# Kernel optimization log

Hardware: AMD Instinct MI355X
Metric: run time of the kernel (lower is better)

Reference implementation:

```python
import jax, jax.numpy as jnp
import numpy as np

E = 1024
H = 16
HD = E // H  # 64


def setup_inputs() -> dict:
    key = jax.random.key(0)
    ks = jax.random.split(key, 5)
    x = jax.random.normal(ks[0], (2, 2048, E), dtype=jnp.float32)
    s = 1.0 / np.sqrt(E)
    W_qkv = jax.random.uniform(ks[1], (E, 3 * E), jnp.float32, -s, s)
    b_qkv = jax.random.uniform(ks[2], (3 * E,), jnp.float32, -s, s)
    W_out = jax.random.uniform(ks[3], (E, E), jnp.float32, -s, s)
    b_out = jax.random.uniform(ks[4], (E,), jnp.float32, -s, s)
    return {"x": x, "W_qkv": W_qkv, "b_qkv": b_qkv, "W_out": W_out, "b_out": b_out}


def reference(x, W_qkv, b_qkv, W_out, b_out):
    B, N, _ = x.shape
    scale = HD ** (-0.5)
    qkv = x @ W_qkv + b_qkv                         # [B, N, 3E]
    qkv = qkv.reshape(B, N, H, 3 * HD)              # torch layout: per-head 3*hd chunk
    qkv = qkv.transpose(0, 2, 1, 3)                 # [B, H, N, 3*hd]
    q, k, v = jnp.split(qkv, 3, axis=-1)            # each [B, H, N, hd]
    attn = jnp.einsum('bhqd,bhkd->bhqk', q, k) * scale
    attn = jax.nn.softmax(attn, axis=-1)            # dropout is identity in eval
    out = jnp.einsum('bhqk,bhkd->bhqd', attn, v)    # [B, H, N, hd]
    out = out.transpose(0, 2, 1, 3).reshape(B, N, E)
    return out @ W_out + b_out
```

## Files before the change

kernel.cpp:

```cpp
#include <hip/hip_runtime.h>


#define SEQ 2048
#define NH  16

typedef __attribute__((ext_vector_type(8))) short short8;
typedef __attribute__((ext_vector_type(4))) short short4v;
typedef __attribute__((ext_vector_type(4))) float floatx4;
typedef __attribute__((ext_vector_type(4))) _Float16 half4;
typedef __attribute__((ext_vector_type(8))) _Float16 half8;
typedef __attribute__((ext_vector_type(2))) _Float16 half2v;
typedef __attribute__((ext_vector_type(2))) __fp16 fp16x2;

#define QSCALE 0.1803368801111204f

__device__ __forceinline__ short f2bf(float f) {
    union { float f; unsigned u; } v; v.f = f;
    unsigned r = v.u + 0x7fffu + ((v.u >> 16) & 1u);
    return (short)(r >> 16);
}

__device__ __forceinline__ float fast_exp2(float x) {
#if __has_builtin(__builtin_amdgcn_exp2f)
    return __builtin_amdgcn_exp2f(x);
#else
    return exp2f(x);
#endif
}

__device__ __forceinline__ half2v cvt_pk(float a, float b) {
#if __has_builtin(__builtin_amdgcn_cvt_pkrtz)
    union { fp16x2 i; half2v o; } u;
    u.i = __builtin_amdgcn_cvt_pkrtz(a, b);
    return u.o;
#else
    half2v r; r.x = (_Float16)a; r.y = (_Float16)b; return r;
#endif
}

#define GLDS16(gp, lp)                                                          \
    __builtin_amdgcn_global_load_lds(                                           \
        (const __attribute__((address_space(1))) unsigned int*)(gp),            \
        (__attribute__((address_space(3))) unsigned int*)(lp), 16, 0, 0)

__global__ __launch_bounds__(256) void prep_kernel(
    const float* __restrict__ x,  short* __restrict__ xb,
    const float* __restrict__ wq, short* __restrict__ wqkvt,
    const float* __restrict__ wo, short* __restrict__ woutt)
{
    const int tid = threadIdx.x;
    const int b = blockIdx.x;
    if (b < 2048) {
        int i = b * 256 + tid;
        const float4* in4 = (const float4*)x + (size_t)i * 2;
        float4 a = in4[0], c = in4[1];
        short8 o = { f2bf(a.x), f2bf(a.y), f2bf(a.z), f2bf(a.w),
                     f2bf(c.x), f2bf(c.y), f2bf(c.z), f2bf(c.w) };
        *((short8*)xb + i) = o;
        return;
    }
    __shared__ float T[64][65];
    const float* in; short* out; int R, C, c0, r0;
    if (b < 2816) {
        int t = b - 2048; in = wq; out = wqkvt; R = 1024; C = 3072;
        c0 = (t % 48) * 64; r0 = (t / 48) * 64;
    } else {
        int t = b - 2816; in = wo; out = woutt; R = 1024; C = 1024;
        c0 = (t & 15) * 64; r0 = (t >> 4) * 64;
    }
#pragma unroll
    for (int it = 0; it < 4; ++it) {
        int r = it * 16 + (tid >> 4), c = (tid & 15) * 4;
        float4 v = *(const float4*)(in + (size_t)(r0 + r) * C + c0 + c);
        T[c+0][r] = v.x; T[c+1][r] = v.y; T[c+2][r] = v.z; T[c+3][r] = v.w;
    }
    __syncthreads();
#pragma unroll
    for (int it = 0; it < 4; ++it) {
        int oc = it * 16 + (tid >> 4), k = (tid & 15) * 4;
        short4v o = { f2bf(T[oc][k]), f2bf(T[oc][k+1]), f2bf(T[oc][k+2]), f2bf(T[oc][k+3]) };
        *(short4v*)(out + (size_t)(c0 + oc) * R + r0 + k) = o;
    }
}

#define GEMM_CORE(A_PTR, B_PTR, LDA, LDB)                                        \
    __shared__ short As[128 * 32];                                               \
    __shared__ short Bs[128 * 32];                                               \
    const int tid  = threadIdx.x;                                                \
    const int lane = tid & 63, w = tid >> 6;                                     \
    const int quad = lane >> 4, l16 = lane & 15;                                 \
    const int wm = w >> 1, wn = w & 1;                                           \
    const int c0 = blockIdx.x * 128, r0 = blockIdx.y * 128;                      \
    floatx4 acc[4][4];                                                           \
    _Pragma("unroll")                                                            \
    for (int i = 0; i < 4; ++i)                                                  \
        _Pragma("unroll")                                                        \
        for (int j = 0; j < 4; ++j) acc[i][j] = (floatx4){0.f, 0.f, 0.f, 0.f};   \
    const int srow = tid >> 2;                                                   \
    const int sgx  = ((tid & 3) ^ ((srow >> 1) & 3)) * 8;                        \
    const short* Ag = (A_PTR) + (size_t)(r0 + srow) * (LDA) + sgx;               \
    const short* Bg = (B_PTR) + (size_t)(c0 + srow) * (LDB) + sgx;               \
    const int fsw = (l16 >> 1) & 3;                                              \
    for (int kk = 0; kk < 1024; kk += 32) {                                      \
        __syncthreads();                                                         \
        GLDS16(Ag + kk,                      As + tid * 8);                      \
        GLDS16(Ag + (size_t)64 * (LDA) + kk, As + 2048 + tid * 8);               \
        GLDS16(Bg + kk,                      Bs + tid * 8);                      \
        GLDS16(Bg + (size_t)64 * (LDB) + kk, Bs + 2048 + tid * 8);               \
        __syncthreads();                                                         \
        short8 af[4], bf[4];                                                     \
        _Pragma("unroll")                                                        \
        for (int mt = 0; mt < 4; ++mt)                                           \
            af[mt] = *(const short8*)&As[(wm * 64 + mt * 16 + l16) * 32 + (quad ^ fsw) * 8]; \
        _Pragma("unroll")                                                        \
        for (int nt = 0; nt < 4; ++nt)                                           \
            bf[nt] = *(const short8*)&Bs[(wn * 64 + nt * 16 + l16) * 32 + (quad ^ fsw) * 8]; \
        _Pragma("unroll")                                                        \
        for (int mt = 0; mt < 4; ++mt)                                           \
            _Pragma("unroll")                                                    \
            for (int nt = 0; nt < 4; ++nt)                                       \
                acc[mt][nt] = __builtin_amdgcn_mfma_f32_16x16x32_bf16(           \
                    af[mt], bf[nt], acc[mt][nt], 0, 0, 0);                       \
    }

__global__ __launch_bounds__(256) void qkv_gemm_kernel(
    const short* __restrict__ wt, const short* __restrict__ xb,
    const float* __restrict__ bias,
    short* __restrict__ qb, short* __restrict__ kb, _Float16* __restrict__ vfb)
{
    GEMM_CORE(wt, xb, 1024, 1024)
#pragma unroll
    for (int mt = 0; mt < 4; ++mt) {
        int oc0 = r0 + wm * 64 + mt * 16 + quad * 4;
        int head = oc0 / 192;
        int t = (oc0 - head * 192) >> 6;
        int d0 = oc0 & 63;
        float4 bv = *(const float4*)(bias + oc0);
#pragma unroll
        for (int nt = 0; nt < 4; ++nt) {
            int tok = c0 + wn * 64 + nt * 16 + l16;
            int bh = (tok >> 11) * NH + head;
            float v0 = acc[mt][nt][0] + bv.x, v1 = acc[mt][nt][1] + bv.y;
            float v2 = acc[mt][nt][2] + bv.z, v3 = acc[mt][nt][3] + bv.w;
            if (t == 2) {
                int n  = tok & (SEQ - 1);
                int h  = nt & 1;
                int qv = l16 >> 2, r = l16 & 3;
                int j  = h * 4 + r;
                size_t vb = (size_t)bh * 131072 + (size_t)(n >> 7) * 8192
                          + (size_t)((n >> 5) & 3) * 2048 + (size_t)d0 * 32 + j;
                _Float16 vv[4] = { (_Float16)v0, (_Float16)v1,
                                   (_Float16)v2, (_Float16)v3 };
#pragma unroll
                for (int jj = 0; jj < 4; ++jj) {
                    int cset = qv ^ (((d0 + jj) >> 1) & 3);
                    vfb[vb + jj * 32 + cset * 8] = vv[jj];
                }
            } else {
                size_t base = ((size_t)bh * SEQ + (tok & (SEQ - 1))) * 64 + d0;
                if (t == 0) {
                    short4v o = { f2bf(v0 * QSCALE), f2bf(v1 * QSCALE),
                                  f2bf(v2 * QSCALE), f2bf(v3 * QSCALE) };
                    *(short4v*)(qb + base) = o;
                } else {
                    short4v o = { f2bf(v0), f2bf(v1), f2bf(v2), f2bf(v3) };
                    *(short4v*)(kb + base) = o;
                }
            }
        }
    }
}

__global__ __launch_bounds__(256) void out_gemm_kernel(
    const short* __restrict__ wt, const short* __restrict__ ab,
    const float* __restrict__ bias, float* __restrict__ out)
{
    __shared__ short As[64 * 32];
    __shared__ short Bs[128 * 32];
    const int tid  = threadIdx.x;
    const int lane = tid & 63, w = tid >> 6;
    const int quad = lane >> 4, l16 = lane & 15;
    const int c0 = blockIdx.x * 128;
    const int r0 = blockIdx.y * 64;
    floatx4 acc[4][2];
#pragma unroll
    for (int i = 0; i < 4; ++i)
#pragma unroll
        for (int j = 0; j < 2; ++j) acc[i][j] = (floatx4){0.f, 0.f, 0.f, 0.f};
    const int srow = tid >> 2;
    const int sgx  = ((tid & 3) ^ ((srow >> 1) & 3)) * 8;
    const short* Ag = wt + (size_t)(r0 + srow) * 1024 + sgx;
    const short* Bg = ab + (size_t)(c0 + srow) * 1024 + sgx;
    const int fsw = (l16 >> 1) & 3;
    for (int kk = 0; kk < 1024; kk += 32) {
        __syncthreads();
        GLDS16(Ag + kk,                   As + tid * 8);
        GLDS16(Bg + kk,                   Bs + tid * 8);
        GLDS16(Bg + (size_t)64 * 1024 + kk, Bs + 2048 + tid * 8);
        __syncthreads();
        short8 af[4], bf[2];
#pragma unroll
        for (int mt = 0; mt < 4; ++mt)
            af[mt] = *(const short8*)&As[(mt * 16 + l16) * 32 + (quad ^ fsw) * 8];
#pragma unroll
        for (int nt = 0; nt < 2; ++nt)
            bf[nt] = *(const short8*)&Bs[(w * 32 + nt * 16 + l16) * 32 + (quad ^ fsw) * 8];
#pragma unroll
        for (int mt = 0; mt < 4; ++mt)
#pragma unroll
            for (int nt = 0; nt < 2; ++nt)
                acc[mt][nt] = __builtin_amdgcn_mfma_f32_16x16x32_bf16(
                    af[mt], bf[nt], acc[mt][nt], 0, 0, 0);
    }
#pragma unroll
    for (int mt = 0; mt < 4; ++mt) {
        int oc0 = r0 + mt * 16 + quad * 4;
        float4 bv = *(const float4*)(bias + oc0);
#pragma unroll
        for (int nt = 0; nt < 2; ++nt) {
            int tok = c0 + w * 32 + nt * 16 + l16;
            float4 o = { acc[mt][nt][0] + bv.x, acc[mt][nt][1] + bv.y,
                         acc[mt][nt][2] + bv.z, acc[mt][nt][3] + bv.w };
            *(float4*)(out + (size_t)tok * 1024 + oc0) = o;
        }
    }
}

__global__ __launch_bounds__(256, 2) void attn_kernel(
    const short* __restrict__ qb, const short* __restrict__ kb,
    const _Float16* __restrict__ vfb, short* __restrict__ ob)
{
    __shared__ short    Ks[128 * 64];
    __shared__ _Float16 Vts[64 * 128];
    const int tid  = threadIdx.x;
    const int lane = tid & 63, w = tid >> 6;
    const int quad = lane >> 4, l16 = lane & 15;
    const int lb = blockIdx.x;
    const int bh = (lb & 7) + (((lb >> 3) & 3) << 3);
    const int q0 = (lb >> 5) * 128;

    short8 aq[2][2];
#pragma unroll
    for (int qf = 0; qf < 2; ++qf) {
        const short* qp = qb + ((size_t)bh * SEQ + q0 + w * 32 + qf * 16 + l16) * 64 + quad * 8;
        aq[qf][0] = *(const short8*)(qp);
        aq[qf][1] = *(const short8*)(qp + 32);
    }

    const int krow = tid >> 3, kg = tid & 7;
    const short* kgp = kb + ((size_t)bh * SEQ + krow) * 64 + (kg ^ (krow & 7)) * 8;
    const short* vgp = (const short*)(vfb + (size_t)bh * 131072) + tid * 8;

    floatx4 o_acc[4][2];
#pragma unroll
    for (int dt = 0; dt < 4; ++dt)
#pragma unroll
        for (int qf = 0; qf < 2; ++qf) o_acc[dt][qf] = (floatx4){0.f, 0.f, 0.f, 0.f};
    float lw[2] = {0.f, 0.f};

    for (int k0 = 0; k0 < SEQ; k0 += 128) {
        __syncthreads();
        const short* kc_p = kgp + (size_t)k0 * 64;
        GLDS16(kc_p,        Ks + tid * 8);
        GLDS16(kc_p + 2048, Ks + 2048 + tid * 8);
        GLDS16(kc_p + 4096, Ks + 4096 + tid * 8);
        GLDS16(kc_p + 6144, Ks + 6144 + tid * 8);
        const short* vc_p = vgp + (size_t)k0 * 64;
        GLDS16(vc_p,        (short*)Vts + tid * 8);
        GLDS16(vc_p + 2048, (short*)Vts + 2048 + tid * 8);
        GLDS16(vc_p + 4096, (short*)Vts + 4096 + tid * 8);
        GLDS16(vc_p + 6144, (short*)Vts + 6144 + tid * 8);
        __syncthreads();

#pragma unroll
        for (int u = 0; u < 4; ++u) {
            half8 av8[4];
#pragma unroll
            for (int dt = 0; dt < 4; ++dt) {
                union { short8 s; half8 h; } vv;
                vv.s = *(const short8*)((const short*)Vts + u * 2048
                        + (dt * 16 + l16) * 32 + (quad ^ ((l16 >> 1) & 3)) * 8);
                av8[dt] = vv.h;
            }
            floatx4 sacc[2][2];
#pragma unroll
            for (int h = 0; h < 2; ++h) {
                const short* krp = &Ks[(u * 32 + h * 16 + l16) * 64];
                short8 ak0 = *(const short8*)(krp + ((0 + quad) ^ (l16 & 7)) * 8);
                short8 ak1 = *(const short8*)(krp + ((4 + quad) ^ (l16 & 7)) * 8);
                __builtin_amdgcn_s_setprio(1);
#pragma unroll
                for (int qf = 0; qf < 2; ++qf) {
                    floatx4 z = (floatx4){0.f, 0.f, 0.f, 0.f};
                    z = __builtin_amdgcn_mfma_f32_16x16x32_bf16(ak0, aq[qf][0], z, 0, 0, 0);
                    sacc[h][qf] = __builtin_amdgcn_mfma_f32_16x16x32_bf16(ak1, aq[qf][1], z, 0, 0, 0);
                }
                __builtin_amdgcn_s_setprio(0);
            }
            half8 pf8[2];
#pragma unroll
            for (int qf = 0; qf < 2; ++qf) {
                float p0 = fast_exp2(sacc[0][qf][0]);
                float p1 = fast_exp2(sacc[0][qf][1]);
                float p2 = fast_exp2(sacc[0][qf][2]);
                float p3 = fast_exp2(sacc[0][qf][3]);
                float p4 = fast_exp2(sacc[1][qf][0]);
                float p5 = fast_exp2(sacc[1][qf][1]);
                float p6 = fast_exp2(sacc[1][qf][2]);
                float p7 = fast_exp2(sacc[1][qf][3]);
                lw[qf] += ((p0 + p1) + (p2 + p3)) + ((p4 + p5) + (p6 + p7));
                half2v a = cvt_pk(p0, p1), b = cvt_pk(p2, p3);
                half2v c = cvt_pk(p4, p5), d = cvt_pk(p6, p7);
                pf8[qf] = (half8){a.x, a.y, b.x, b.y, c.x, c.y, d.x, d.y};
            }
            __builtin_amdgcn_s_setprio(1);
#pragma unroll
            for (int dt = 0; dt < 4; ++dt)
#pragma unroll
                for (int qf = 0; qf < 2; ++qf)
                    o_acc[dt][qf] = __builtin_amdgcn_mfma_f32_16x16x32_f16(
                        av8[dt], pf8[qf], o_acc[dt][qf], 0, 0, 0);
            __builtin_amdgcn_s_setprio(0);
        }
    }

    float inv[2];
#pragma unroll
    for (int qf = 0; qf < 2; ++qf) {
        lw[qf] += __shfl_xor(lw[qf], 16);
        lw[qf] += __shfl_xor(lw[qf], 32);
        inv[qf] = 1.0f / lw[qf];
    }

    const int b = bh >> 4, h = bh & 15;
#pragma unroll
    for (int dt = 0; dt < 4; ++dt)
#pragma unroll
        for (int qf = 0; qf < 2; ++qf) {
            int tok = b * SEQ + q0 + w * 32 + qf * 16 + l16;
            floatx4 o = o_acc[dt][qf];
            short4v o4 = { f2bf(o[0] * inv[qf]), f2bf(o[1] * inv[qf]),
                           f2bf(o[2] * inv[qf]), f2bf(o[3] * inv[qf]) };
            *(short4v*)(ob + (size_t)tok * 1024 + h * 64 + dt * 16 + quad * 4) = o4;
        }
}

extern "C" void kernel_launch(void* const* d_in, const int* in_sizes, int n_in,
                              void* d_out, int out_size, void* d_ws, size_t ws_size,
                              hipStream_t stream) {
    const float* x     = (const float*)d_in[0];
    const float* W_qkv = (const float*)d_in[1];
    const float* b_qkv = (const float*)d_in[2];
    const float* W_out = (const float*)d_in[3];
    const float* b_out = (const float*)d_in[4];
    float* out = (float*)d_out;

    short* xb      = (short*)d_ws;
    short* wqkvt   = xb    + (size_t)4096 * 1024;
    short* woutt   = wqkvt + (size_t)3072 * 1024;
    short* qb      = woutt + (size_t)1024 * 1024;
    short* kb      = qb    + (size_t)32 * SEQ * 64;
    _Float16* vfb  = (_Float16*)(kb + (size_t)32 * SEQ * 64);
    short* ob      = (short*)(vfb + (size_t)32 * 64 * SEQ);

    prep_kernel<<<3072, 256, 0, stream>>>(x, xb, W_qkv, wqkvt, W_out, woutt);
    qkv_gemm_kernel<<<dim3(32, 24), 256, 0, stream>>>(wqkvt, xb, b_qkv, qb, kb, vfb);
    attn_kernel<<<512, 256, 0, stream>>>(qb, kb, vfb, ob);
    out_gemm_kernel<<<dim3(32, 16), 256, 0, stream>>>(woutt, ob, b_out, out);
}
```

Before: 174.3 us.

## Double-buffer K/V tiles in shared memory to overlap loads with compute

The attention kernel now keeps two shared-memory buffers for K and V tiles. It issues the global-to-LDS loads for the next 128-key tile before computing on the current one, leaving one barrier per iteration instead of two. This is meant to hide global load latency behind the MFMA work. LDS use doubles to 64KB per block, which may cut occupancy below the 2 blocks per CU the launch bounds request. The barrier at the end of each iteration may also not wait on the outstanding async LDS loads unless GLDS16 or the barrier drains vmcnt.

After: 174.0 us, median of 2. No clear change (-0.1%).

```diff
diff --git a/kernel.cpp b/kernel.cpp
--- a/kernel.cpp
+++ b/kernel.cpp
@@ -230,8 +230,8 @@
     const short* __restrict__ qb, const short* __restrict__ kb,
     const _Float16* __restrict__ vfb, short* __restrict__ ob)
 {
-    __shared__ short    Ks[128 * 64];
-    __shared__ _Float16 Vts[64 * 128];
+    __shared__ short    Ks[2][128 * 64];
+    __shared__ _Float16 Vts[2][64 * 128];
     const int tid  = threadIdx.x;
     const int lane = tid & 63, w = tid >> 6;
     const int quad = lane >> 4, l16 = lane & 15;
@@ -258,34 +258,51 @@
         for (int qf = 0; qf < 2; ++qf) o_acc[dt][qf] = (floatx4){0.f, 0.f, 0.f, 0.f};
     float lw[2] = {0.f, 0.f};
 
+    {
+        GLDS16(kgp,        &Ks[0][0] + tid * 8);
+        GLDS16(kgp + 2048, &Ks[0][0] + 2048 + tid * 8);
+        GLDS16(kgp + 4096, &Ks[0][0] + 4096 + tid * 8);
+        GLDS16(kgp + 6144, &Ks[0][0] + 6144 + tid * 8);
+        GLDS16(vgp,        (short*)&Vts[0][0] + tid * 8);
+        GLDS16(vgp + 2048, (short*)&Vts[0][0] + 2048 + tid * 8);
+        GLDS16(vgp + 4096, (short*)&Vts[0][0] + 4096 + tid * 8);
+        GLDS16(vgp + 6144, (short*)&Vts[0][0] + 6144 + tid * 8);
+    }
+    __syncthreads();
+
+    int cur = 0;
     for (int k0 = 0; k0 < SEQ; k0 += 128) {
-        __syncthreads();
-        const short* kc_p = kgp + (size_t)k0 * 64;
-        GLDS16(kc_p,        Ks + tid * 8);
-        GLDS16(kc_p + 2048, Ks + 2048 + tid * 8);
-        GLDS16(kc_p + 4096, Ks + 4096 + tid * 8);
-        GLDS16(kc_p + 6144, Ks + 6144 + tid * 8);
-        const short* vc_p = vgp + (size_t)k0 * 64;
-        GLDS16(vc_p,        (short*)Vts + tid * 8);
-        GLDS16(vc_p + 2048, (short*)Vts + 2048 + tid * 8);
-        GLDS16(vc_p + 4096, (short*)Vts + 4096 + tid * 8);
-        GLDS16(vc_p + 6144, (short*)Vts + 6144 + tid * 8);
-        __syncthreads();
-
+        if (k0 + 128 < SEQ) {
+            const short* kn = kgp + (size_t)(k0 + 128) * 64;
+            short* kd = &Ks[cur ^ 1][0];
+            GLDS16(kn,        kd + tid * 8);
+            GLDS16(kn + 2048, kd + 2048 + tid * 8);
+            GLDS16(kn + 4096, kd + 4096 + tid * 8);
+            GLDS16(kn + 6144, kd + 6144 + tid * 8);
+            const short* vn = vgp + (size_t)(k0 + 128) * 64;
+            short* vd = (short*)&Vts[cur ^ 1][0];
+            GLDS16(vn,        vd + tid * 8);
+            GLDS16(vn + 2048, vd + 2048 + tid * 8);
+            GLDS16(vn + 4096, vd + 4096 + tid * 8);
+            GLDS16(vn + 6144, vd + 6144 + tid * 8);
+        }
+
+        const short* ksc = &Ks[cur][0];
+        const short* vsc = (const short*)&Vts[cur][0];
 #pragma unroll
         for (int u = 0; u < 4; ++u) {
             half8 av8[4];
 #pragma unroll
             for (int dt = 0; dt < 4; ++dt) {
                 union { short8 s; half8 h; } vv;
-                vv.s = *(const short8*)((const short*)Vts + u * 2048
+                vv.s = *(const short8*)(vsc + u * 2048
                         + (dt * 16 + l16) * 32 + (quad ^ ((l16 >> 1) & 3)) * 8);
                 av8[dt] = vv.h;
             }
             floatx4 sacc[2][2];
 #pragma unroll
             for (int h = 0; h < 2; ++h) {
-                const short* krp = &Ks[(u * 32 + h * 16 + l16) * 64];
+                const short* krp = ksc + (u * 32 + h * 16 + l16) * 64;
                 short8 ak0 = *(const short8*)(krp + ((0 + quad) ^ (l16 & 7)) * 8);
                 short8 ak1 = *(const short8*)(krp + ((4 + quad) ^ (l16 & 7)) * 8);
                 __builtin_amdgcn_s_setprio(1);
@@ -322,6 +339,9 @@
                         av8[dt], pf8[qf], o_acc[dt][qf], 0, 0, 0);
             __builtin_amdgcn_s_setprio(0);
         }
+
+        __syncthreads();
+        cur ^= 1;
     }
 
     float inv[2];
```
